# Performance work log

Hardware: AMD Instinct MI355X
Metric: run time of the kernel (lower is better)

## Reference

```python
import jax, jax.numpy as jnp
import numpy as np

D_MODEL = 512
NUM_HEADS = 8
D_K = D_MODEL // NUM_HEADS


def setup_inputs() -> dict:
    key = jax.random.key(0)
    kx, kq, kk, kv, ko = jax.random.split(key, 5)
    scale = 1.0 / np.sqrt(D_MODEL)
    return {
        "x": jax.random.normal(kx, (2, 4096, D_MODEL), dtype=jnp.float32),
        "Wq": jax.random.normal(kq, (D_MODEL, D_MODEL), dtype=jnp.float32) * scale,
        "Wk": jax.random.normal(kk, (D_MODEL, D_MODEL), dtype=jnp.float32) * scale,
        "Wv": jax.random.normal(kv, (D_MODEL, D_MODEL), dtype=jnp.float32) * scale,
        "Wo": jax.random.normal(ko, (D_MODEL, D_MODEL), dtype=jnp.float32) * scale,
    }


def reference(x, Wq, Wk, Wv, Wo):
    B, T, D = x.shape
    H, dk = NUM_HEADS, D_K
    # Linear(d,d, bias=False): y = x @ W.T ; weights stored [out,in] like torch
    q = (x @ Wq.T).reshape(B, T, H, dk).transpose(0, 2, 1, 3)  # [B,H,T,dk]
    k = (x @ Wk.T).reshape(B, T, H, dk).transpose(0, 2, 1, 3)
    v = (x @ Wv.T).reshape(B, T, H, dk).transpose(0, 2, 1, 3)
    scores = jnp.einsum("bhqd,bhkd->bhqk", q, k) / np.sqrt(dk)  # [B,H,T,T]
    probs = jax.nn.softmax(scores, axis=-1)
    o = jnp.einsum("bhqk,bhkd->bhqd", probs, v)  # [B,H,T,dk]
    o = o.transpose(0, 2, 1, 3).reshape(B, T, D)
    return o @ Wo.T
```

## Files before the change

### kernel.cpp

```cpp
#include <hip/hip_runtime.h>
#include <hip/hip_bf16.h>

#define SEQ 4096
#define DMODEL 512
#define HEADS 8
#define DK 64
#define BATCH 2
#define MTOT (BATCH * SEQ)
#define NBH (BATCH * HEADS)

typedef __attribute__((ext_vector_type(8))) short bh8;
typedef __attribute__((ext_vector_type(4))) float f4;
typedef __attribute__((ext_vector_type(16))) float f16x;
typedef __attribute__((ext_vector_type(2))) float f2;

union uf { f16x v; f2 h[8]; };

#define MFMA(a, b, c)   __builtin_amdgcn_mfma_f32_16x16x32_bf16(a, b, c, 0, 0, 0)
#define MFMA32(a, b, c) __builtin_amdgcn_mfma_f32_32x32x16_bf16(a, b, c, 0, 0, 0)
#define GLL16(g, l) __builtin_amdgcn_global_load_lds( \
    (const __attribute__((address_space(1))) void*)(g), \
    (__attribute__((address_space(3))) void*)(l), 16, 0, 0)

__device__ __forceinline__ unsigned short f2b(float f) {
    union { float f; unsigned u; } v; v.f = f;
    unsigned r = v.u + 0x7fff + ((v.u >> 16) & 1);
    return (unsigned short)(r >> 16);
}

__device__ __forceinline__ unsigned cvtpk(float lo, float hi) {
    unsigned r;
    asm("v_cvt_pk_bf16_f32 %0, %1, %2" : "=v"(r) : "v"(lo), "v"(hi));
    return r;
}
__device__ __forceinline__ void plswap(unsigned& a, unsigned& b) {
    asm("v_permlane32_swap_b32 %0, %1" : "+v"(a), "+v"(b));
}
__device__ __forceinline__ float wave_max_pair(float x) {
    float b = x; asm("" : "+v"(b));
    float a = x;
    asm("v_permlane32_swap_b32 %0, %1" : "+v"(a), "+v"(b));
    return fmaxf(a, b);
}
__device__ __forceinline__ float wave_sum_pair(float x) {
    float b = x; asm("" : "+v"(b));
    float a = x;
    asm("v_permlane32_swap_b32 %0, %1" : "+v"(a), "+v"(b));
    return a + b;
}
__device__ __forceinline__ f2 pk_add(f2 a, f2 b) {
    f2 d; asm("v_pk_add_f32 %0, %1, %2" : "=v"(d) : "v"(a), "v"(b)); return d;
}
__device__ __forceinline__ f2 pk_mul(f2 a, f2 b) {
    f2 d; asm("v_pk_mul_f32 %0, %1, %2" : "=v"(d) : "v"(a), "v"(b)); return d;
}
__device__ __forceinline__ float max3f(float a, float b, float c) {
    float d; asm("v_max3_f32 %0, %1, %2, %3" : "=v"(d) : "v"(a), "v"(b), "v"(c));
    return d;
}

__global__ __launch_bounds__(256) void convert_k(
    const float* __restrict__ x, const float* __restrict__ wq,
    const float* __restrict__ wk, const float* __restrict__ wv,
    const float* __restrict__ wo, unsigned short* __restrict__ dst)
{
    const size_t i = ((size_t)blockIdx.x * 256 + threadIdx.x) * 4;
    const float* s; size_t o;
    if (i < 4194304u)                 { s = x;  o = i; }
    else if (i < 4194304u + 262144u)  { s = wq; o = i - 4194304u; }
    else if (i < 4194304u + 524288u)  { s = wk; o = i - (4194304u + 262144u); }
    else if (i < 4194304u + 786432u)  { s = wv; o = i - (4194304u + 524288u); }
    else                              { s = wo; o = i - (4194304u + 786432u); }
    float4 v = *(const float4*)(s + o);
    ushort4 u; u.x = f2b(v.x); u.y = f2b(v.y); u.z = f2b(v.z); u.w = f2b(v.w);
    *(ushort4*)(dst + i) = u;
}

__global__ __launch_bounds__(256) void qkv_gemm_mfma(
    const unsigned short* __restrict__ xb,
    const unsigned short* __restrict__ Wb,
    unsigned short* __restrict__ QKV)
{
    const int z = blockIdx.z;
    const unsigned short* A = xb;
    const unsigned short* B = Wb + (size_t)z * (DMODEL * DMODEL);
    const int m0 = blockIdx.x * 128, n0 = blockIdx.y * 128;
    const int tid = threadIdx.x, w = tid >> 6, l = tid & 63;
    const int wr = w >> 1, wc = w & 1;

    __shared__ __align__(16) unsigned short As[128 * 32];
    __shared__ __align__(16) unsigned short Bs[128 * 32];

    f4 acc[4][4] = {};
    const int lrow = l >> 2, lslot = l & 3;

    for (int k0 = 0; k0 < DMODEL; k0 += 32) {
        __syncthreads();
        #pragma unroll
        for (int j = 0; j < 2; ++j) {
            const int row = w * 32 + j * 16 + lrow;
            const int sw = lslot ^ ((row >> 1) & 3);
            GLL16(A + (size_t)(m0 + row) * DMODEL + k0 + sw * 8,
                  (char*)As + (w * 32 + j * 16) * 64);
            GLL16(B + (size_t)(n0 + row) * DMODEL + k0 + sw * 8,
                  (char*)Bs + (w * 32 + j * 16) * 64);
        }
        __syncthreads();
        bh8 af[4], bg[4];
        #pragma unroll
        for (int mi = 0; mi < 4; ++mi) {
            const int r = wr * 64 + mi * 16 + (l & 15);
            af[mi] = *(const bh8*)((const char*)As + r * 64 +
                                   (((l >> 4) * 16) ^ (((r >> 1) & 3) << 4)));
        }
        #pragma unroll
        for (int ni = 0; ni < 4; ++ni) {
            const int r = wc * 64 + ni * 16 + (l & 15);
            bg[ni] = *(const bh8*)((const char*)Bs + r * 64 +
                                   (((l >> 4) * 16) ^ (((r >> 1) & 3) << 4)));
        }
        #pragma unroll
        for (int mi = 0; mi < 4; ++mi)
            #pragma unroll
            for (int ni = 0; ni < 4; ++ni)
                acc[mi][ni] = MFMA(af[mi], bg[ni], acc[mi][ni]);
    }

    unsigned short* Out = QKV + (size_t)z * ((size_t)NBH * SEQ * DK);
    const float sc = (z == 0) ? 0.18033688011112042f : 1.0f;
    #pragma unroll
    for (int mi = 0; mi < 4; ++mi) {
        #pragma unroll
        for (int rg = 0; rg < 4; ++rg) {
            const int m = m0 + wr * 64 + mi * 16 + (l >> 4) * 4 + rg;
            const int b = m >> 12, t = m & (SEQ - 1);
            #pragma unroll
            for (int ni = 0; ni < 4; ++ni) {
                const int n = n0 + wc * 64 + ni * 16 + (l & 15);
                const int h = n >> 6, d = n & 63;
                Out[(((size_t)(b * HEADS + h)) * SEQ + t) * DK + d] =
                    f2b(acc[mi][ni][rg] * sc);
            }
        }
    }
}

__global__ __launch_bounds__(256) void vtrans(
    const unsigned short* __restrict__ Vh, unsigned short* __restrict__ Vt)
{
    const int bh = blockIdx.y, t0 = blockIdx.x * 64;
    __shared__ unsigned short L[64][72];
    const unsigned short* src = Vh + ((size_t)bh * SEQ + t0) * DK;
    const int r = threadIdx.x >> 3, c8 = (threadIdx.x & 7) * 8;
    #pragma unroll
    for (int it = 0; it < 2; ++it) {
        const int row = r + it * 32;
        ushort4 a = *(const ushort4*)(src + (size_t)row * DK + c8);
        ushort4 b = *(const ushort4*)(src + (size_t)row * DK + c8 + 4);
        L[row][c8 + 0] = a.x; L[row][c8 + 1] = a.y; L[row][c8 + 2] = a.z; L[row][c8 + 3] = a.w;
        L[row][c8 + 4] = b.x; L[row][c8 + 5] = b.y; L[row][c8 + 6] = b.z; L[row][c8 + 7] = b.w;
    }
    __syncthreads();
    unsigned short* dst = Vt + (size_t)bh * DK * SEQ + t0;
    #pragma unroll
    for (int it = 0; it < 2; ++it) {
        const int d = r + it * 32;
        ushort4 a, b;
        a.x = L[c8 + 0][d]; a.y = L[c8 + 1][d]; a.z = L[c8 + 2][d]; a.w = L[c8 + 3][d];
        b.x = L[c8 + 4][d]; b.y = L[c8 + 5][d]; b.z = L[c8 + 6][d]; b.w = L[c8 + 7][d];
        *(ushort4*)(dst + (size_t)d * SEQ + c8) = a;
        *(ushort4*)(dst + (size_t)d * SEQ + c8 + 4) = b;
    }
}

__global__ __launch_bounds__(512, 2) void flash_mfma(
    const unsigned short* __restrict__ Qh,
    const unsigned short* __restrict__ Kh,
    const unsigned short* __restrict__ Vtp,
    unsigned short* __restrict__ Ow)
{
    const int bid = blockIdx.x;
    const int bh = bid & 15, q0 = (bid >> 4) * 256;
    const int tid = threadIdx.x, w = tid >> 6, l = tid & 63;
    const int lq = l & 31, hi = l >> 5;

    __shared__ __align__(16) char lds[65536];

    const unsigned short* Qb = Qh + (size_t)bh * SEQ * DK;
    const unsigned short* Kb = Kh + (size_t)bh * SEQ * DK;
    const unsigned short* Vb = Vtp + (size_t)bh * DK * SEQ;

    bh8 qf[4];
    #pragma unroll
    for (int ks = 0; ks < 4; ++ks)
        qf[ks] = *(const bh8*)(Qb + (size_t)(q0 + w * 32 + lq) * DK + ks * 16 + hi * 8);

    const int koff = ((w >> 2) * 32 + lq) * DK + (w & 3) * 16 + hi * 8;
    const int voff = ((w >> 2) * 32 + lq) * SEQ + (w & 3) * 16 + hi * 8;

    f16x oA0 = {}, oA1 = {}, oB0 = {}, oB1 = {};
    float mA = -3.0e38f, lA = 0.f, mB = -3.0e38f, lB = 0.f;

#define STAGE(buf_, half_, kv0_) do {                                         \
    GLL16(Kb + (size_t)(half_) * (2048 * DK) + (size_t)(kv0_) * DK + koff,    \
          lds + (buf_) * 32768 + (half_) * 16384 + w * 1024);                 \
    GLL16(Vb + (half_) * 2048 + (size_t)(kv0_) + voff,                        \
          lds + (buf_) * 32768 + (half_) * 16384 + 8192 + w * 1024);          \
} while (0)

#define QKT(kb_, sa0_, sa1_) do {                                             \
    __builtin_amdgcn_s_setprio(1);                                            \
    _Pragma("unroll")                                                         \
    for (int ks_ = 0; ks_ < 4; ++ks_) {                                       \
        bh8 k0_ = *(const bh8*)((kb_) + ks_ * 1024);                          \
        bh8 k1_ = *(const bh8*)((kb_) + (4 + ks_) * 1024);                    \
        sa0_ = MFMA32(k0_, qf[ks_], sa0_);                                    \
        sa1_ = MFMA32(k1_, qf[ks_], sa1_);                                    \
    }                                                                         \
    __builtin_amdgcn_s_setprio(0);                                            \
} while (0)

#define SMPV(kb_, sa0_, sa1_, m_run_, l_run_, o0_, o1_) do {                  \
    float a_ = fmaxf(sa0_[0], sa0_[1]);                                       \
    float b_ = fmaxf(sa1_[0], sa1_[1]);                                       \
    _Pragma("unroll")                                                         \
    for (int r_ = 2; r_ < 16; r_ += 2) {                                      \
        a_ = max3f(a_, sa0_[r_], sa0_[r_ + 1]);                               \
        b_ = max3f(b_, sa1_[r_], sa1_[r_ + 1]);                               \
    }                                                                         \
    const float mx_ = wave_max_pair(fmaxf(a_, b_));                           \
    const bool skip_ = __all(mx_ <= m_run_ + 8.0f);                           \
    float mnew_ = m_run_, corr_ = 1.0f;                                       \
    if (!skip_) {                                                             \
        mnew_ = fmaxf(m_run_, mx_);                                           \
        corr_ = __builtin_amdgcn_exp2f(m_run_ - mnew_);                       \
    }                                                                         \
    uf U0_, U1_; U0_.v = sa0_; U1_.v = sa1_;                                  \
    f2 nm2_; nm2_[0] = -mnew_; nm2_[1] = -mnew_;                              \
    f2 p2_[16];                                                               \
    _Pragma("unroll")                                                         \
    for (int i_ = 0; i_ < 8; ++i_) {                                          \
        f2 t0_ = pk_add(U0_.h[i_], nm2_);                                     \
        f2 t1_ = pk_add(U1_.h[i_], nm2_);                                     \
        f2 e0_, e1_;                                                          \
        e0_[0] = __builtin_amdgcn_exp2f(t0_[0]);                              \
        e0_[1] = __builtin_amdgcn_exp2f(t0_[1]);                              \
        e1_[0] = __builtin_amdgcn_exp2f(t1_[0]);                              \
        e1_[1] = __builtin_amdgcn_exp2f(t1_[1]);                              \
        p2_[i_] = e0_; p2_[8 + i_] = e1_;                                     \
    }                                                                         \
    f2 s0_ = pk_add(p2_[0], p2_[1]),   s1_ = pk_add(p2_[2], p2_[3]);          \
    f2 s2_ = pk_add(p2_[4], p2_[5]),   s3_ = pk_add(p2_[6], p2_[7]);          \
    f2 s4_ = pk_add(p2_[8], p2_[9]),   s5_ = pk_add(p2_[10], p2_[11]);        \
    f2 s6_ = pk_add(p2_[12], p2_[13]), s7_ = pk_add(p2_[14], p2_[15]);        \
    s0_ = pk_add(s0_, s1_); s2_ = pk_add(s2_, s3_);                           \
    s4_ = pk_add(s4_, s5_); s6_ = pk_add(s6_, s7_);                           \
    s0_ = pk_add(s0_, s2_); s4_ = pk_add(s4_, s6_);                           \
    s0_ = pk_add(s0_, s4_);                                                   \
    const float psum_ = wave_sum_pair(s0_[0] + s0_[1]);                       \
    if (!skip_) {                                                             \
        m_run_ = mnew_;                                                       \
        l_run_ = l_run_ * corr_ + psum_;                                      \
        f2 c2_; c2_[0] = corr_; c2_[1] = corr_;                               \
        uf O0_, O1_; O0_.v = o0_; O1_.v = o1_;                                \
        _Pragma("unroll")                                                     \
        for (int i_ = 0; i_ < 8; ++i_) {                                      \
            O0_.h[i_] = pk_mul(O0_.h[i_], c2_);                               \
            O1_.h[i_] = pk_mul(O1_.h[i_], c2_);                               \
        }                                                                     \
        o0_ = O0_.v; o1_ = O1_.v;                                             \
    } else {                                                                  \
        l_run_ += psum_;                                                      \
    }                                                                         \
    bh8 pf_[4];                                                               \
    _Pragma("unroll")                                                         \
    for (int cb_ = 0; cb_ < 2; ++cb_) {                                       \
        unsigned k0_ = cvtpk(p2_[8 * cb_ + 0][0], p2_[8 * cb_ + 0][1]);       \
        unsigned k1_ = cvtpk(p2_[8 * cb_ + 1][0], p2_[8 * cb_ + 1][1]);       \
        unsigned k2_ = cvtpk(p2_[8 * cb_ + 2][0], p2_[8 * cb_ + 2][1]);       \
        unsigned k3_ = cvtpk(p2_[8 * cb_ + 3][0], p2_[8 * cb_ + 3][1]);       \
        unsigned k4_ = cvtpk(p2_[8 * cb_ + 4][0], p2_[8 * cb_ + 4][1]);       \
        unsigned k5_ = cvtpk(p2_[8 * cb_ + 5][0], p2_[8 * cb_ + 5][1]);       \
        unsigned k6_ = cvtpk(p2_[8 * cb_ + 6][0], p2_[8 * cb_ + 6][1]);       \
        unsigned k7_ = cvtpk(p2_[8 * cb_ + 7][0], p2_[8 * cb_ + 7][1]);       \
        plswap(k0_, k2_); plswap(k1_, k3_); plswap(k4_, k6_); plswap(k5_, k7_);\
        union { unsigned u[4]; bh8 v; } f0_, f1_;                             \
        f0_.u[0] = k0_; f0_.u[1] = k1_; f0_.u[2] = k2_; f0_.u[3] = k3_;       \
        f1_.u[0] = k4_; f1_.u[1] = k5_; f1_.u[2] = k6_; f1_.u[3] = k7_;       \
        pf_[cb_ * 2 + 0] = f0_.v;                                             \
        pf_[cb_ * 2 + 1] = f1_.v;                                             \
    }                                                                         \
    const char* vb_ = (kb_) + 8192;                                           \
    __builtin_amdgcn_s_setprio(1);                                            \
    _Pragma("unroll")                                                         \
    for (int ks_ = 0; ks_ < 4; ++ks_) {                                       \
        bh8 v0_ = *(const bh8*)(vb_ + ks_ * 1024);                            \
        bh8 v1_ = *(const bh8*)(vb_ + (4 + ks_) * 1024);                      \
        o0_ = MFMA32(v0_, pf_[ks_], o0_);                                     \
        o1_ = MFMA32(v1_, pf_[ks_], o1_);                                     \
    }                                                                         \
    __builtin_amdgcn_s_setprio(0);                                            \
} while (0)

    STAGE(0, 0, 0);
    STAGE(0, 1, 0);
    __syncthreads();
    int cur = 0;
    const char* myfrag = lds + l * 16;

    for (int t = 0; t < 32; ++t) {
        if (t < 31) {
            STAGE(cur ^ 1, 0, (t + 1) * 64);
            STAGE(cur ^ 1, 1, (t + 1) * 64);
        }

        const char* kbA = myfrag + cur * 32768;
        const char* kbB = kbA + 16384;

        f16x sA0 = {}, sA1 = {}, sB0 = {}, sB1 = {};
        QKT(kbA, sA0, sA1);
        QKT(kbB, sB0, sB1);
        SMPV(kbA, sA0, sA1, mA, lA, oA0, oA1);
        SMPV(kbB, sB0, sB1, mB, lB, oB0, oB1);

        __syncthreads();
        cur ^= 1;
    }
#undef STAGE
#undef QKT
#undef SMPV

    const float mt = fmaxf(mA, mB);
    const float cA = __builtin_amdgcn_exp2f(mA - mt);
    const float cB = __builtin_amdgcn_exp2f(mB - mt);
    f16x o0, o1;
    #pragma unroll
    for (int r = 0; r < 16; ++r) {
        o0[r] = oA0[r] * cA + oB0[r] * cB;
        o1[r] = oA1[r] * cA + oB1[r] * cB;
    }
    const float inv = 1.0f / (lA * cA + lB * cB);

    char* Tb = lds + w * 4096;
    #pragma unroll
    for (int db = 0; db < 2; ++db) {
        f16x ov = db ? o1 : o0;
        #pragma unroll
        for (int j = 0; j < 8; ++j) {
            const int r = 2 * j;
            const int d = db * 32 + (r & 3) + 8 * (r >> 2) + 4 * hi;
            unsigned pk = cvtpk(ov[r] * inv, ov[r + 1] * inv);
            *(unsigned*)(Tb + lq * 128 + ((d * 2) ^ ((lq & 7) << 4))) = pk;
        }
    }
    __syncthreads();
    const int b = bh >> 3, h = bh & 7;
    const int row = l >> 1, half = l & 1;
    const int q = q0 + w * 32 + row;
    unsigned short* dst = Ow + ((size_t)b * SEQ + q) * DMODEL + h * DK + half * 32;
    #pragma unroll
    for (int i = 0; i < 4; ++i) {
        const int byte = (half * 64 + i * 16) ^ ((row & 7) << 4);
        uint4 vv = *(const uint4*)(Tb + row * 128 + byte);
        *(uint4*)(dst + i * 8) = vv;
    }
}

__global__ __launch_bounds__(256) void out_gemm_mfma(
    const unsigned short* __restrict__ Ob,
    const unsigned short* __restrict__ Wob,
    float* __restrict__ out)
{
    const int m0 = blockIdx.x * 128, n0 = blockIdx.y * 128;
    const int tid = threadIdx.x, w = tid >> 6, l = tid & 63;
    const int wr = w >> 1, wc = w & 1;

    __shared__ __align__(16) unsigned short As[128 * 32];
    __shared__ __align__(16) unsigned short Bs[128 * 32];

    f4 acc[4][4] = {};
    const int lrow = l >> 2, lslot = l & 3;

    for (int k0 = 0; k0 < DMODEL; k0 += 32) {
        __syncthreads();
        #pragma unroll
        for (int j = 0; j < 2; ++j) {
            const int row = w * 32 + j * 16 + lrow;
            const int sw = lslot ^ ((row >> 1) & 3);
            GLL16(Ob + (size_t)(m0 + row) * DMODEL + k0 + sw * 8,
                  (char*)As + (w * 32 + j * 16) * 64);
            GLL16(Wob + (size_t)(n0 + row) * DMODEL + k0 + sw * 8,
                  (char*)Bs + (w * 32 + j * 16) * 64);
        }
        __syncthreads();
        bh8 af[4], bg[4];
        #pragma unroll
        for (int mi = 0; mi < 4; ++mi) {
            const int r = wr * 64 + mi * 16 + (l & 15);
            af[mi] = *(const bh8*)((const char*)As + r * 64 +
                                   (((l >> 4) * 16) ^ (((r >> 1) & 3) << 4)));
        }
        #pragma unroll
        for (int ni = 0; ni < 4; ++ni) {
            const int r = wc * 64 + ni * 16 + (l & 15);
            bg[ni] = *(const bh8*)((const char*)Bs + r * 64 +
                                   (((l >> 4) * 16) ^ (((r >> 1) & 3) << 4)));
        }
        #pragma unroll
        for (int mi = 0; mi < 4; ++mi)
            #pragma unroll
            for (int ni = 0; ni < 4; ++ni)
                acc[mi][ni] = MFMA(af[mi], bg[ni], acc[mi][ni]);
    }

    #pragma unroll
    for (int mi = 0; mi < 4; ++mi) {
        #pragma unroll
        for (int rg = 0; rg < 4; ++rg) {
            const int m = m0 + wr * 64 + mi * 16 + (l >> 4) * 4 + rg;
            #pragma unroll
            for (int ni = 0; ni < 4; ++ni) {
                const int n = n0 + wc * 64 + ni * 16 + (l & 15);
                out[(size_t)m * DMODEL + n] = acc[mi][ni][rg];
            }
        }
    }
}

extern "C" void kernel_launch(void* const* d_in, const int* in_sizes, int n_in,
                              void* d_out, int out_size, void* d_ws, size_t ws_size,
                              hipStream_t stream)
{
    const float* x  = (const float*)d_in[0];
    const float* Wq = (const float*)d_in[1];
    const float* Wk = (const float*)d_in[2];
    const float* Wv = (const float*)d_in[3];
    const float* Wo = (const float*)d_in[4];
    float* out = (float*)d_out;

    unsigned short* ws = (unsigned short*)d_ws;
    unsigned short* xb  = ws;
    unsigned short* Wb  = xb + 4194304;
    unsigned short* QKV = Wb + 4 * 262144;
    unsigned short* Vt  = QKV + 3 * 4194304;
    unsigned short* Ow  = Vt + 4194304;
    unsigned short* Qh = QKV;
    unsigned short* Kh = QKV + 4194304;
    unsigned short* Vh = QKV + 2 * 4194304;

    convert_k<<<5120, 256, 0, stream>>>(x, Wq, Wk, Wv, Wo, ws);
    qkv_gemm_mfma<<<dim3(MTOT / 128, DMODEL / 128, 3), 256, 0, stream>>>(xb, Wb, QKV);
    vtrans<<<dim3(SEQ / 64, NBH), 256, 0, stream>>>(Vh, Vt);
    flash_mfma<<<256, 512, 0, stream>>>(Qh, Kh, Vt, Ow);
    out_gemm_mfma<<<dim3(MTOT / 128, DMODEL / 128), 256, 0, stream>>>(
        Ow, Wb + 3 * 262144, out);
}
```

Before: 134.2 us.

## Split attention KV range across two blocks and merge partials in a new kernel

The flash attention grid doubles from 256 to 512 blocks: each block now covers half of the key/value sequence and writes unnormalized bf16 partial outputs plus per-row max and sum. A new merge kernel rescales and combines the two partials, normalizes them and writes the head-interleaved output for the final projection. This aims to raise occupancy on a GPU where 256 large blocks left compute units underused. The cost is an extra launch, extra global traffic for the partials, and some bf16 rounding of unnormalized partial sums. Buffers that are no longer needed are reused to hold the partials.

```diff
diff --git a/kernel.cpp b/kernel.cpp
--- a/kernel.cpp
+++ b/kernel.cpp
@@ -26,6 +26,12 @@
     union { float f; unsigned u; } v; v.f = f;
     unsigned r = v.u + 0x7fff + ((v.u >> 16) & 1);
     return (unsigned short)(r >> 16);
+}
+__device__ __forceinline__ float lo2f(unsigned u) {
+    union { unsigned u; float f; } v; v.u = u << 16; return v.f;
+}
+__device__ __forceinline__ float hi2f(unsigned u) {
+    union { unsigned u; float f; } v; v.u = u & 0xffff0000u; return v.f;
 }
 
 __device__ __forceinline__ unsigned cvtpk(float lo, float hi) {
@@ -177,12 +183,16 @@
     const unsigned short* __restrict__ Qh,
     const unsigned short* __restrict__ Kh,
     const unsigned short* __restrict__ Vtp,
-    unsigned short* __restrict__ Ow)
+    unsigned short* __restrict__ P0,
+    unsigned short* __restrict__ P1,
+    float* __restrict__ MLp)
 {
     const int bid = blockIdx.x;
-    const int bh = bid & 15, q0 = (bid >> 4) * 256;
+    const int bh = bid & 15, qt = (bid >> 4) & 15, kvp = bid >> 8;
+    const int q0 = qt * 256;
     const int tid = threadIdx.x, w = tid >> 6, l = tid & 63;
     const int lq = l & 31, hi = l >> 5;
+    const int kvbase = kvp * 2048;
 
     __shared__ __align__(16) char lds[65536];
 
@@ -202,9 +212,9 @@
     float mA = -3.0e38f, lA = 0.f, mB = -3.0e38f, lB = 0.f;
 
 #define STAGE(buf_, half_, kv0_) do {                                         \
-    GLL16(Kb + (size_t)(half_) * (2048 * DK) + (size_t)(kv0_) * DK + koff,    \
+    GLL16(Kb + (size_t)(kvbase + (half_) * 1024 + (kv0_)) * DK + koff,        \
           lds + (buf_) * 32768 + (half_) * 16384 + w * 1024);                 \
-    GLL16(Vb + (half_) * 2048 + (size_t)(kv0_) + voff,                        \
+    GLL16(Vb + (size_t)(kvbase + (half_) * 1024 + (kv0_)) + voff,             \
           lds + (buf_) * 32768 + (half_) * 16384 + 8192 + w * 1024);          \
 } while (0)
 
@@ -308,8 +318,8 @@
     int cur = 0;
     const char* myfrag = lds + l * 16;
 
-    for (int t = 0; t < 32; ++t) {
-        if (t < 31) {
+    for (int t = 0; t < 16; ++t) {
+        if (t < 15) {
             STAGE(cur ^ 1, 0, (t + 1) * 64);
             STAGE(cur ^ 1, 1, (t + 1) * 64);
         }
@@ -339,7 +349,7 @@
         o0[r] = oA0[r] * cA + oB0[r] * cB;
         o1[r] = oA1[r] * cA + oB1[r] * cB;
     }
-    const float inv = 1.0f / (lA * cA + lB * cB);
+    const float l_tot = lA * cA + lB * cB;
 
     char* Tb = lds + w * 4096;
     #pragma unroll
@@ -349,20 +359,69 @@
         for (int j = 0; j < 8; ++j) {
             const int r = 2 * j;
             const int d = db * 32 + (r & 3) + 8 * (r >> 2) + 4 * hi;
-            unsigned pk = cvtpk(ov[r] * inv, ov[r + 1] * inv);
+            unsigned pk = cvtpk(ov[r], ov[r + 1]);
             *(unsigned*)(Tb + lq * 128 + ((d * 2) ^ ((lq & 7) << 4))) = pk;
         }
     }
     __syncthreads();
-    const int b = bh >> 3, h = bh & 7;
+    unsigned short* po = kvp ? P1 : P0;
     const int row = l >> 1, half = l & 1;
-    const int q = q0 + w * 32 + row;
-    unsigned short* dst = Ow + ((size_t)b * SEQ + q) * DMODEL + h * DK + half * 32;
+    const int qloc = w * 32 + row;
+    unsigned short* dst = po + (((size_t)bh * 16 + qt) * 256 + qloc) * 64 + half * 32;
     #pragma unroll
     for (int i = 0; i < 4; ++i) {
         const int byte = (half * 64 + i * 16) ^ ((row & 7) << 4);
-        uint4 vv = *(const uint4*)(Tb + row * 128 + byte);
-        *(uint4*)(dst + i * 8) = vv;
+        *(uint4*)(dst + i * 8) = *(const uint4*)(Tb + row * 128 + byte);
+    }
+    if (hi == 0) {
+        float* mlb = MLp + (((size_t)kvp * 16 + bh) * 16 + qt) * 512;
+        mlb[w * 32 + lq] = mt;
+        mlb[256 + w * 32 + lq] = l_tot;
+    }
+}
+
+__global__ __launch_bounds__(512) void merge_k(
+    const unsigned short* __restrict__ P0,
+    const unsigned short* __restrict__ P1,
+    const float* __restrict__ MLp,
+    unsigned short* __restrict__ Ow)
+{
+    const int qt = blockIdx.x, bh = blockIdx.y;
+    const int tid = threadIdx.x;
+    __shared__ float C0[256], C1[256];
+    if (tid < 256) {
+        const float* m0b = MLp + (((size_t)bh) * 16 + qt) * 512;
+        const float* m1b = MLp + (((size_t)16 + bh) * 16 + qt) * 512;
+        const float m0 = m0b[tid], l0 = m0b[256 + tid];
+        const float m1 = m1b[tid], l1 = m1b[256 + tid];
+        const float m = fmaxf(m0, m1);
+        const float c0 = __builtin_amdgcn_exp2f(m0 - m);
+        const float c1 = __builtin_amdgcn_exp2f(m1 - m);
+        const float inv = 1.0f / (l0 * c0 + l1 * c1);
+        C0[tid] = c0 * inv;
+        C1[tid] = c1 * inv;
+    }
+    __syncthreads();
+    const int q = tid >> 1, half = tid & 1;
+    const float c0 = C0[q], c1 = C1[q];
+    const size_t off = (((size_t)bh * 16 + qt) * 256 + q) * 64 + half * 32;
+    const int b = bh >> 3, h = bh & 7;
+    unsigned short* dst = Ow + ((size_t)b * SEQ + qt * 256 + q) * DMODEL + h * DK + half * 32;
+    #pragma unroll
+    for (int i = 0; i < 4; ++i) {
+        uint4 a = *(const uint4*)(P0 + off + i * 8);
+        uint4 bb = *(const uint4*)(P1 + off + i * 8);
+        uint4 o;
+        unsigned* ap = (unsigned*)&a;
+        unsigned* bp = (unsigned*)&bb;
+        unsigned* op = (unsigned*)&o;
+        #pragma unroll
+        for (int k = 0; k < 4; ++k) {
+            const unsigned ua = ap[k], ub = bp[k];
+            op[k] = cvtpk(lo2f(ua) * c0 + lo2f(ub) * c1,
+                          hi2f(ua) * c0 + hi2f(ub) * c1);
+        }
+        *(uint4*)(dst + i * 8) = o;
     }
 }
 
@@ -448,10 +507,15 @@
     unsigned short* Kh = QKV + 4194304;
     unsigned short* Vh = QKV + 2 * 4194304;
 
+    unsigned short* P0 = xb;
+    unsigned short* P1 = Vh;
+    float* MLp = (float*)Wb;
+
     convert_k<<<5120, 256, 0, stream>>>(x, Wq, Wk, Wv, Wo, ws);
     qkv_gemm_mfma<<<dim3(MTOT / 128, DMODEL / 128, 3), 256, 0, stream>>>(xb, Wb, QKV);
     vtrans<<<dim3(SEQ / 64, NBH), 256, 0, stream>>>(Vh, Vt);
-    flash_mfma<<<256, 512, 0, stream>>>(Qh, Kh, Vt, Ow);
+    flash_mfma<<<512, 512, 0, stream>>>(Qh, Kh, Vt, P0, P1, MLp);
+    merge_k<<<dim3(16, 16), 512, 0, stream>>>(P0, P1, MLp, Ow);
     out_gemm_mfma<<<dim3(MTOT / 128, DMODEL / 128), 256, 0, stream>>>(
         Ow, Wb + 3 * 262144, out);
 }
```

Measured after the change: 146.0 us. 1.09x slower.
